# Performance work log

Hardware: AMD Instinct MI355X
Metric: run time of the kernel (lower is better)

## Reference

```python
import math
import jax, jax.numpy as jnp
import numpy as np

H = 16       # num_attention_heads
HD = 64      # head_size
D = H * HD   # hidden_size = 1024
B = 4
L = 1024
P = 2 * L - 1  # relative position length


def setup_inputs() -> dict:
    key = jax.random.key(0)
    ks = jax.random.split(key, 12)
    s = 0.02
    return {
        "hidden_states": jax.random.normal(ks[0], (B, L, D), jnp.float32),
        "relative_position_embeddings": jax.random.normal(ks[1], (1, P, D), jnp.float32),
        "Wq": jax.random.normal(ks[2], (D, D), jnp.float32) * s,
        "bq": jnp.zeros((D,), jnp.float32),
        "Wk": jax.random.normal(ks[3], (D, D), jnp.float32) * s,
        "bk": jnp.zeros((D,), jnp.float32),
        "Wv": jax.random.normal(ks[4], (D, D), jnp.float32) * s,
        "bv": jnp.zeros((D,), jnp.float32),
        "Wpos": jax.random.normal(ks[5], (D, D), jnp.float32) * s,  # linear_pos, no bias
        "pos_bias_u": jax.random.normal(ks[6], (H, HD), jnp.float32) * s,
        "pos_bias_v": jax.random.normal(ks[7], (H, HD), jnp.float32) * s,
        "Wo": jax.random.normal(ks[8], (D, D), jnp.float32) * s,
        "bo": jnp.zeros((D,), jnp.float32),
    }


def reference(hidden_states, relative_position_embeddings, Wq, bq, Wk, bk, Wv, bv,
              Wpos, pos_bias_u, pos_bias_v, Wo, bo):
    b, l, d = hidden_states.shape
    scale = 1.0 / math.sqrt(HD)

    # QKV projections -> [B, L, H, HD]
    q = (hidden_states @ Wq + bq).reshape(b, l, H, HD)
    k = (hidden_states @ Wk + bk).reshape(b, l, H, HD)
    v = (hidden_states @ Wv + bv).reshape(b, l, H, HD)

    # projected relative position embeddings -> [P, H, HD]
    pos = (relative_position_embeddings[0] @ Wpos).reshape(-1, H, HD)
    p = pos.shape[0]

    # Transformer-XL style content/position scores
    q_u = q + pos_bias_u  # [B, L, H, HD]
    q_v = q + pos_bias_v
    scores_ac = jnp.einsum('blhd,bmhd->bhlm', q_u, k)      # [B, H, L, L]
    scores_bd = jnp.einsum('blhd,phd->bhlp', q_v, pos)     # [B, H, L, P]

    # relative shift trick: pad one zero column, reshape, drop first row, re-slice
    zero_pad = jnp.zeros((b, H, l, 1), scores_bd.dtype)
    sbd = jnp.concatenate([zero_pad, scores_bd], axis=-1)  # [B, H, L, P+1]
    sbd = sbd.reshape(b, H, p + 1, l)[:, :, 1:]            # [B, H, P, L]
    sbd = sbd.reshape(b, H, l, p)[..., : p // 2 + 1]       # [B, H, L, L]

    scores = (scores_ac + sbd) * scale
    probs = jax.nn.softmax(scores, axis=-1)                # dropout p=0 (eval)

    ctx = jnp.einsum('bhlm,bmhd->blhd', probs, v).reshape(b, l, d)
    out = ctx @ Wo + bo
    return (out, probs)
```

## Files before the change

kernel.cpp:

```cpp
#include <hip/hip_runtime.h>
#include <hip/hip_bf16.h>

constexpr int H  = 16;
constexpr int HD = 64;
constexpr int D  = 1024;
constexpr int B  = 4;
constexpr int L  = 1024;
constexpr int P  = 2047;
constexpr int Pp = 2048;
constexpr int M  = B * L;
constexpr long OUT_ELEMS = (long)B * L * D;
constexpr float SCALE = 0.125f;

typedef __attribute__((ext_vector_type(8))) short  bf16x8;
typedef __attribute__((ext_vector_type(4))) float  f32x4;

#define MFMA(a, b, c) __builtin_amdgcn_mfma_f32_16x16x32_bf16((a), (b), (c), 0, 0, 0)

__device__ __forceinline__ unsigned short f2bf(float f) {
    __hip_bfloat16 h = __float2bfloat16(f);
    return __builtin_bit_cast(unsigned short, h);
}
__device__ __forceinline__ float bf2f(unsigned short u) {
    unsigned int v = ((unsigned int)u) << 16;
    return __builtin_bit_cast(float, v);
}

__global__ void cvt_kernel(const float* __restrict__ in, unsigned short* __restrict__ out,
                           long nvalid, long ntotal) {
    long i = ((long)blockIdx.x * blockDim.x + threadIdx.x) * 4;
    if (i >= ntotal) return;
    if (i < nvalid) {
        float4 v = *(const float4*)(in + i);
        out[i + 0] = f2bf(v.x);
        out[i + 1] = f2bf(v.y);
        out[i + 2] = f2bf(v.z);
        out[i + 3] = f2bf(v.w);
    } else {
        out[i + 0] = 0; out[i + 1] = 0; out[i + 2] = 0; out[i + 3] = 0;
    }
}

__global__ void wtrans_kernel(const float* __restrict__ W, unsigned short* __restrict__ Wt) {
    __shared__ float t[32][33];
    int n0 = blockIdx.x * 32, k0 = blockIdx.y * 32;
    int tx = threadIdx.x, ty = threadIdx.y;
#pragma unroll
    for (int s = 0; s < 4; ++s)
        t[ty + s * 8][tx] = W[(long)(k0 + ty + s * 8) * D + n0 + tx];
    __syncthreads();
#pragma unroll
    for (int s = 0; s < 4; ++s)
        Wt[(long)(n0 + ty + s * 8) * D + k0 + tx] = f2bf(t[tx][ty + s * 8]);
}

__global__ void vtrans_kernel(const unsigned short* __restrict__ Vb, unsigned short* __restrict__ Vt) {
    __shared__ unsigned short t[64][65];
    int b = blockIdx.z, h = blockIdx.y, l0 = blockIdx.x * 64;
    int tx = threadIdx.x & 63, ty = threadIdx.x >> 6;
#pragma unroll
    for (int s = 0; s < 16; ++s) {
        int l = s * 4 + ty;
        t[l][tx] = Vb[(long)(b * L + l0 + l) * D + h * HD + tx];
    }
    __syncthreads();
#pragma unroll
    for (int s = 0; s < 16; ++s) {
        int d = s * 4 + ty;
        Vt[(long)((b * H + h) * HD + d) * L + l0 + tx] = t[tx][d];
    }
}

template <int MODE>
__global__ __launch_bounds__(256) void gemm_bt(const unsigned short* __restrict__ A,
                                               const unsigned short* __restrict__ Bt,
                                               const float* __restrict__ bias,
                                               float* __restrict__ outF,
                                               unsigned short* __restrict__ outB) {
    int wave = threadIdx.x >> 6;
    int lane = threadIdx.x & 63;
    int r = lane & 15, g = lane >> 4;
    int row0 = blockIdx.x * 64 + wave * 16;
    int col0 = blockIdx.y * 64;
    f32x4 acc[4] = {};
    const long arow = (long)(row0 + r) * D;
    for (int ks = 0; ks < D; ks += 32) {
        bf16x8 a = *(const bf16x8*)(A + arow + ks + g * 8);
#pragma unroll
        for (int c = 0; c < 4; ++c) {
            bf16x8 b = *(const bf16x8*)(Bt + (long)(col0 + c * 16 + r) * D + ks + g * 8);
            acc[c] = MFMA(a, b, acc[c]);
        }
    }
#pragma unroll
    for (int c = 0; c < 4; ++c) {
        int col = col0 + c * 16 + r;
        float bv = (MODE != 2) ? bias[col] : 0.f;
#pragma unroll
        for (int i = 0; i < 4; ++i) {
            long row = row0 + g * 4 + i;
            float v = acc[c][i] + bv;
            if (MODE == 0) outF[row * D + col] = v;
            else           outB[row * D + col] = f2bf(v);
        }
    }
}

template <int OUT>
__device__ __forceinline__ void attn_sweep(
    int b, int h, int l0, int r, int g,
    const bf16x8* aqu, const bf16x8* aqv,
    const unsigned short* __restrict__ Kb, const unsigned short* __restrict__ posb,
    const unsigned short* __restrict__ Vt,
    float (*Es)[80], unsigned short* Ps,
    float* rsum, const float* inv, float* __restrict__ probs, f32x4* ctxacc)
{
    const long Srow0 = ((long)((b * H + h) * L + l0)) * L;
    for (int mc = 0; mc < L; mc += 64) {
        int rp0 = (L - 1) + mc - l0 - 15;
        f32x4 eacc[5];
#pragma unroll
        for (int t = 0; t < 5; ++t) eacc[t] = f32x4{0.f, 0.f, 0.f, 0.f};
#pragma unroll
        for (int ks = 0; ks < 2; ++ks)
#pragma unroll
            for (int t = 0; t < 5; ++t) {
                bf16x8 bp = *(const bf16x8*)(posb + (long)(rp0 + t * 16 + r) * D + h * HD + ks * 32 + g * 8);
                eacc[t] = MFMA(aqv[ks], bp, eacc[t]);
            }
#pragma unroll
        for (int t = 0; t < 5; ++t)
#pragma unroll
            for (int i = 0; i < 4; ++i)
                Es[g * 4 + i][t * 16 + r] = eacc[t][i];
        asm volatile("s_waitcnt lgkmcnt(0)" ::: "memory");
        __builtin_amdgcn_sched_barrier(0);

#pragma unroll
        for (int t = 0; t < 4; ++t) {
            f32x4 acc = {0.f, 0.f, 0.f, 0.f};
#pragma unroll
            for (int ks = 0; ks < 2; ++ks) {
                bf16x8 bk = *(const bf16x8*)(Kb + (long)(b * L + mc + t * 16 + r) * D + h * HD + ks * 32 + g * 8);
                acc = MFMA(aqu[ks], bk, acc);
            }
            int j = t * 16 + r;
#pragma unroll
            for (int i = 0; i < 4; ++i) {
                int il = g * 4 + i;
                float s = (acc[i] + Es[il][j - il + 15]) * SCALE;
                float e = __expf(s);
                if (OUT) {
                    float p = e * inv[i];
                    probs[Srow0 + (long)il * L + mc + j] = p;
                    int elem = il * 64 + j;
                    Ps[elem ^ ((il & 7) << 3)] = f2bf(p);
                } else {
                    rsum[i] += e;
                }
            }
        }
        if (OUT) {
            asm volatile("s_waitcnt lgkmcnt(0)" ::: "memory");
            __builtin_amdgcn_sched_barrier(0);
#pragma unroll
            for (int kh = 0; kh < 2; ++kh) {
                int elem = (r * 64 + kh * 32 + g * 8) ^ ((r & 7) << 3);
                bf16x8 pa = *(const bf16x8*)(Ps + elem);
#pragma unroll
                for (int c = 0; c < 4; ++c) {
                    bf16x8 bv = *(const bf16x8*)(Vt + (long)((b * H + h) * HD + c * 16 + r) * L + mc + kh * 32 + g * 8);
                    ctxacc[c] = MFMA(pa, bv, ctxacc[c]);
                }
            }
        }
        asm volatile("" ::: "memory");
    }
}

__global__ __launch_bounds__(256) void fused_attn(
    const unsigned short* __restrict__ Qb, const unsigned short* __restrict__ Kb,
    const unsigned short* __restrict__ posb, const float* __restrict__ pu,
    const float* __restrict__ pv, const unsigned short* __restrict__ Vt,
    float* __restrict__ probs, unsigned short* __restrict__ ctxb)
{
    __shared__ float Es[4][16][80];
    __shared__ unsigned short Ps[4][1024];
    int tid = threadIdx.x;
    int wave = tid >> 6, lane = tid & 63;
    int r = lane & 15, g = lane >> 4;

    int lin = blockIdx.x;
    int swz = (lin & 7) * 128 + (lin >> 3);
    int h = swz >> 6;
    int b = (swz >> 4) & 3;
    int l0 = (swz & 15) * 64 + wave * 16;

    bf16x8 aqu[2], aqv[2];
    long qoff = (long)(b * L + l0 + r) * D + h * HD;
#pragma unroll
    for (int ks = 0; ks < 2; ++ks) {
        bf16x8 q = *(const bf16x8*)(Qb + qoff + ks * 32 + g * 8);
        bf16x8 u, v;
#pragma unroll
        for (int e = 0; e < 8; ++e) {
            float qf = bf2f((unsigned short)q[e]);
            int d = ks * 32 + g * 8 + e;
            u[e] = (short)f2bf(qf + pu[h * HD + d]);
            v[e] = (short)f2bf(qf + pv[h * HD + d]);
        }
        aqu[ks] = u; aqv[ks] = v;
    }

    float rsum[4] = {0.f, 0.f, 0.f, 0.f};
    f32x4 ctxacc[4] = {};

    attn_sweep<0>(b, h, l0, r, g, aqu, aqv, Kb, posb, Vt,
                  Es[wave], Ps[wave], rsum, nullptr, probs, ctxacc);

    float inv[4];
#pragma unroll
    for (int i = 0; i < 4; ++i) {
        float s = rsum[i];
        for (int off = 1; off < 16; off <<= 1) s += __shfl_xor(s, off);
        inv[i] = 1.0f / s;
    }

    attn_sweep<1>(b, h, l0, r, g, aqu, aqv, Kb, posb, Vt,
                  Es[wave], Ps[wave], rsum, inv, probs, ctxacc);

#pragma unroll
    for (int c = 0; c < 4; ++c)
#pragma unroll
        for (int i = 0; i < 4; ++i)
            ctxb[(long)(b * L + l0 + g * 4 + i) * D + h * HD + c * 16 + r] = f2bf(ctxacc[c][i]);
}

extern "C" void kernel_launch(void* const* d_in, const int* in_sizes, int n_in,
                              void* d_out, int out_size, void* d_ws, size_t ws_size,
                              hipStream_t stream) {
    const float* hs   = (const float*)d_in[0];
    const float* rpe  = (const float*)d_in[1];
    const float* Wq   = (const float*)d_in[2];
    const float* bq   = (const float*)d_in[3];
    const float* Wk   = (const float*)d_in[4];
    const float* bk   = (const float*)d_in[5];
    const float* Wv   = (const float*)d_in[6];
    const float* bv   = (const float*)d_in[7];
    const float* Wpos = (const float*)d_in[8];
    const float* pu   = (const float*)d_in[9];
    const float* pv   = (const float*)d_in[10];
    const float* Wo   = (const float*)d_in[11];
    const float* bo   = (const float*)d_in[12];

    char* ws = (char*)d_ws;
    size_t off = 0;
    auto alloc = [&](size_t bytes) -> void* {
        void* p = ws + off;
        off += (bytes + 255) & ~(size_t)255;
        return p;
    };
    unsigned short* Xb   = (unsigned short*)alloc((size_t)M * D * 2);
    unsigned short* Wqt  = (unsigned short*)alloc((size_t)D * D * 2);
    unsigned short* Wkt  = (unsigned short*)alloc((size_t)D * D * 2);
    unsigned short* Wvt  = (unsigned short*)alloc((size_t)D * D * 2);
    unsigned short* Wpot = (unsigned short*)alloc((size_t)D * D * 2);
    unsigned short* Wot  = (unsigned short*)alloc((size_t)D * D * 2);
    unsigned short* rpb  = (unsigned short*)alloc((size_t)Pp * D * 2);
    unsigned short* posb = (unsigned short*)alloc((size_t)Pp * D * 2);
    unsigned short* Qb   = (unsigned short*)alloc((size_t)M * D * 2);
    unsigned short* Kb   = (unsigned short*)alloc((size_t)M * D * 2);
    unsigned short* Vb   = (unsigned short*)alloc((size_t)M * D * 2);
    unsigned short* Vt   = (unsigned short*)alloc((size_t)M * D * 2);
    unsigned short* ctxb = (unsigned short*)alloc((size_t)M * D * 2);

    float* outp  = (float*)d_out;
    float* probs = outp + OUT_ELEMS;

    cvt_kernel<<<(M * D) / 1024, 256, 0, stream>>>(hs, Xb, (long)M * D, (long)M * D);
    cvt_kernel<<<(Pp * D) / 1024, 256, 0, stream>>>(rpe, rpb, (long)P * D, (long)Pp * D);
    dim3 wtg(32, 32), wtb(32, 8);
    wtrans_kernel<<<wtg, wtb, 0, stream>>>(Wq, Wqt);
    wtrans_kernel<<<wtg, wtb, 0, stream>>>(Wk, Wkt);
    wtrans_kernel<<<wtg, wtb, 0, stream>>>(Wv, Wvt);
    wtrans_kernel<<<wtg, wtb, 0, stream>>>(Wpos, Wpot);
    wtrans_kernel<<<wtg, wtb, 0, stream>>>(Wo, Wot);

    gemm_bt<1><<<dim3(M / 64, D / 64), 256, 0, stream>>>(Xb, Wqt, bq, nullptr, Qb);
    gemm_bt<1><<<dim3(M / 64, D / 64), 256, 0, stream>>>(Xb, Wkt, bk, nullptr, Kb);
    gemm_bt<1><<<dim3(M / 64, D / 64), 256, 0, stream>>>(Xb, Wvt, bv, nullptr, Vb);
    gemm_bt<2><<<dim3(Pp / 64, D / 64), 256, 0, stream>>>(rpb, Wpot, nullptr, nullptr, posb);
    vtrans_kernel<<<dim3(L / 64, H, B), 256, 0, stream>>>(Vb, Vt);

    fused_attn<<<B * H * (L / 64), 256, 0, stream>>>(Qb, Kb, posb, pu, pv, Vt, probs, ctxb);

    gemm_bt<0><<<dim3(M / 64, D / 64), 256, 0, stream>>>(ctxb, Wot, bo, outp, nullptr);
}
```

Baseline: 1.036 ms.

## Split attention key range across four waves and cache exp values between passes

```diff
diff --git a/kernel.cpp b/kernel.cpp
--- a/kernel.cpp
+++ b/kernel.cpp
@@ -106,134 +106,184 @@
     }
 }
 
-template <int OUT>
-__device__ __forceinline__ void attn_sweep(
-    int b, int h, int l0, int r, int g,
-    const bf16x8* aqu, const bf16x8* aqv,
-    const unsigned short* __restrict__ Kb, const unsigned short* __restrict__ posb,
-    const unsigned short* __restrict__ Vt,
-    float (*Es)[80], unsigned short* Ps,
-    float* rsum, const float* inv, float* __restrict__ probs, f32x4* ctxacc)
-{
-    const long Srow0 = ((long)((b * H + h) * L + l0)) * L;
-    for (int mc = 0; mc < L; mc += 64) {
-        int rp0 = (L - 1) + mc - l0 - 15;
-        f32x4 eacc[5];
-#pragma unroll
-        for (int t = 0; t < 5; ++t) eacc[t] = f32x4{0.f, 0.f, 0.f, 0.f};
-#pragma unroll
-        for (int ks = 0; ks < 2; ++ks)
-#pragma unroll
-            for (int t = 0; t < 5; ++t) {
-                bf16x8 bp = *(const bf16x8*)(posb + (long)(rp0 + t * 16 + r) * D + h * HD + ks * 32 + g * 8);
-                eacc[t] = MFMA(aqv[ks], bp, eacc[t]);
-            }
-#pragma unroll
-        for (int t = 0; t < 5; ++t)
-#pragma unroll
-            for (int i = 0; i < 4; ++i)
-                Es[g * 4 + i][t * 16 + r] = eacc[t][i];
-        asm volatile("s_waitcnt lgkmcnt(0)" ::: "memory");
-        __builtin_amdgcn_sched_barrier(0);
-
-#pragma unroll
-        for (int t = 0; t < 4; ++t) {
-            f32x4 acc = {0.f, 0.f, 0.f, 0.f};
-#pragma unroll
-            for (int ks = 0; ks < 2; ++ks) {
-                bf16x8 bk = *(const bf16x8*)(Kb + (long)(b * L + mc + t * 16 + r) * D + h * HD + ks * 32 + g * 8);
-                acc = MFMA(aqu[ks], bk, acc);
-            }
-            int j = t * 16 + r;
-#pragma unroll
-            for (int i = 0; i < 4; ++i) {
-                int il = g * 4 + i;
-                float s = (acc[i] + Es[il][j - il + 15]) * SCALE;
-                float e = __expf(s);
-                if (OUT) {
-                    float p = e * inv[i];
-                    probs[Srow0 + (long)il * L + mc + j] = p;
-                    int elem = il * 64 + j;
-                    Ps[elem ^ ((il & 7) << 3)] = f2bf(p);
-                } else {
-                    rsum[i] += e;
-                }
-            }
-        }
-        if (OUT) {
-            asm volatile("s_waitcnt lgkmcnt(0)" ::: "memory");
-            __builtin_amdgcn_sched_barrier(0);
-#pragma unroll
-            for (int kh = 0; kh < 2; ++kh) {
-                int elem = (r * 64 + kh * 32 + g * 8) ^ ((r & 7) << 3);
-                bf16x8 pa = *(const bf16x8*)(Ps + elem);
-#pragma unroll
-                for (int c = 0; c < 4; ++c) {
-                    bf16x8 bv = *(const bf16x8*)(Vt + (long)((b * H + h) * HD + c * 16 + r) * L + mc + kh * 32 + g * 8);
-                    ctxacc[c] = MFMA(pa, bv, ctxacc[c]);
-                }
-            }
-        }
-        asm volatile("" ::: "memory");
-    }
-}
-
-__global__ __launch_bounds__(256) void fused_attn(
+__global__ __launch_bounds__(1024, 4) void fused_attn(
     const unsigned short* __restrict__ Qb, const unsigned short* __restrict__ Kb,
     const unsigned short* __restrict__ posb, const float* __restrict__ pu,
     const float* __restrict__ pv, const unsigned short* __restrict__ Vt,
     float* __restrict__ probs, unsigned short* __restrict__ ctxb)
 {
-    __shared__ float Es[4][16][80];
-    __shared__ unsigned short Ps[4][1024];
+    __shared__ __align__(16) unsigned short scratch[16][1600];
+    __shared__ __align__(16) float rs[64][4];
+    __shared__ __align__(16) float ctxcomb[4][16][68];
+
     int tid = threadIdx.x;
     int wave = tid >> 6, lane = tid & 63;
     int r = lane & 15, g = lane >> 4;
+    int wq = wave & 3, wr = wave >> 2;
 
     int lin = blockIdx.x;
     int swz = (lin & 7) * 128 + (lin >> 3);
     int h = swz >> 6;
     int b = (swz >> 4) & 3;
-    int l0 = (swz & 15) * 64 + wave * 16;
+    int l0base = (swz & 15) * 64;
+    int l0 = l0base + wr * 16;
+
+    unsigned short* Es = scratch[wave];
+    unsigned short* Ps = scratch[wave];
+    const int hHD = h * HD;
 
     bf16x8 aqu[2], aqv[2];
-    long qoff = (long)(b * L + l0 + r) * D + h * HD;
-#pragma unroll
-    for (int ks = 0; ks < 2; ++ks) {
-        bf16x8 q = *(const bf16x8*)(Qb + qoff + ks * 32 + g * 8);
-        bf16x8 u, v;
-#pragma unroll
-        for (int e = 0; e < 8; ++e) {
-            float qf = bf2f((unsigned short)q[e]);
-            int d = ks * 32 + g * 8 + e;
-            u[e] = (short)f2bf(qf + pu[h * HD + d]);
-            v[e] = (short)f2bf(qf + pv[h * HD + d]);
-        }
-        aqu[ks] = u; aqv[ks] = v;
+    {
+        long qoff = (long)(b * L + l0 + r) * D + hHD;
+#pragma unroll
+        for (int ks = 0; ks < 2; ++ks) {
+            bf16x8 q = *(const bf16x8*)(Qb + qoff + ks * 32 + g * 8);
+            bf16x8 u, v;
+#pragma unroll
+            for (int e = 0; e < 8; ++e) {
+                float qf = bf2f((unsigned short)q[e]);
+                int d = ks * 32 + g * 8 + e;
+                u[e] = (short)f2bf(qf + pu[hHD + d]);
+                v[e] = (short)f2bf(qf + pv[hHD + d]);
+            }
+            aqu[ks] = u; aqv[ks] = v;
+        }
     }
 
     float rsum[4] = {0.f, 0.f, 0.f, 0.f};
-    f32x4 ctxacc[4] = {};
-
-    attn_sweep<0>(b, h, l0, r, g, aqu, aqv, Kb, posb, Vt,
-                  Es[wave], Ps[wave], rsum, nullptr, probs, ctxacc);
-
-    float inv[4];
+    unsigned int pPk[4][4][2];
+    const long KbRow = (long)(b * L) * D + hHD;
+
+#pragma unroll
+    for (int cc = 0; cc < 4; ++cc) {
+        int mc = wq * 256 + cc * 64;
+        int rp0 = (L - 1) + mc - l0 - 15;
+        f32x4 eacc[5] = {};
+#pragma unroll
+        for (int ks = 0; ks < 2; ++ks)
+#pragma unroll
+            for (int t = 0; t < 5; ++t) {
+                bf16x8 bp = *(const bf16x8*)(posb + (long)(rp0 + t * 16 + r) * D + hHD + ks * 32 + g * 8);
+                eacc[t] = MFMA(aqv[ks], bp, eacc[t]);
+            }
+#pragma unroll
+        for (int t = 0; t < 5; ++t) {
+            ushort4 pk;
+            pk.x = f2bf(eacc[t][0]); pk.y = f2bf(eacc[t][1]);
+            pk.z = f2bf(eacc[t][2]); pk.w = f2bf(eacc[t][3]);
+            *(ushort4*)(Es + (t * 16 + r) * 20 + g * 4) = pk;
+        }
+        asm volatile("s_waitcnt lgkmcnt(0)" ::: "memory");
+        __builtin_amdgcn_sched_barrier(0);
+
+#pragma unroll
+        for (int t = 0; t < 4; ++t) {
+            f32x4 acc = {};
+#pragma unroll
+            for (int ks = 0; ks < 2; ++ks) {
+                bf16x8 bk = *(const bf16x8*)(Kb + KbRow + (long)(mc + t * 16 + r) * D + ks * 32 + g * 8);
+                acc = MFMA(aqu[ks], bk, acc);
+            }
+            float ev[4];
+#pragma unroll
+            for (int i = 0; i < 4; ++i) {
+                int il = g * 4 + i;
+                int c = t * 16 + r - il + 15;
+                float s = (acc[i] + bf2f(Es[c * 20 + il])) * SCALE;
+                float e = __expf(s);
+                rsum[i] += e;
+                ev[i] = e;
+            }
+            pPk[cc][t][0] = ((unsigned)f2bf(ev[1]) << 16) | f2bf(ev[0]);
+            pPk[cc][t][1] = ((unsigned)f2bf(ev[3]) << 16) | f2bf(ev[2]);
+        }
+        asm volatile("" ::: "memory");
+    }
+
 #pragma unroll
     for (int i = 0; i < 4; ++i) {
         float s = rsum[i];
-        for (int off = 1; off < 16; off <<= 1) s += __shfl_xor(s, off);
-        inv[i] = 1.0f / s;
-    }
-
-    attn_sweep<1>(b, h, l0, r, g, aqu, aqv, Kb, posb, Vt,
-                  Es[wave], Ps[wave], rsum, inv, probs, ctxacc);
-
-#pragma unroll
-    for (int c = 0; c < 4; ++c)
-#pragma unroll
-        for (int i = 0; i < 4; ++i)
-            ctxb[(long)(b * L + l0 + g * 4 + i) * D + h * HD + c * 16 + r] = f2bf(ctxacc[c][i]);
+        s += __shfl_xor(s, 1); s += __shfl_xor(s, 2);
+        s += __shfl_xor(s, 4); s += __shfl_xor(s, 8);
+        rsum[i] = s;
+    }
+    if (r == 0) {
+#pragma unroll
+        for (int i = 0; i < 4; ++i) rs[wr * 16 + g * 4 + i][wq] = rsum[i];
+    }
+    __syncthreads();
+    float inv[4];
+#pragma unroll
+    for (int i = 0; i < 4; ++i) {
+        float4 v = *(const float4*)&rs[wr * 16 + g * 4 + i][0];
+        inv[i] = 1.0f / (v.x + v.y + v.z + v.w);
+    }
+
+    f32x4 ctxacc[4] = {};
+    const long ProwBase = ((long)((b * H + h) * L + l0)) * L;
+    const long VtBase = (long)((b * H + h) * HD) * L;
+#pragma unroll
+    for (int cc = 0; cc < 4; ++cc) {
+        int mc = wq * 256 + cc * 64;
+#pragma unroll
+        for (int t = 0; t < 4; ++t) {
+            float ev[4];
+            ev[0] = bf2f((unsigned short)(pPk[cc][t][0] & 0xffff));
+            ev[1] = bf2f((unsigned short)(pPk[cc][t][0] >> 16));
+            ev[2] = bf2f((unsigned short)(pPk[cc][t][1] & 0xffff));
+            ev[3] = bf2f((unsigned short)(pPk[cc][t][1] >> 16));
+#pragma unroll
+            for (int i = 0; i < 4; ++i) {
+                int il = g * 4 + i;
+                int j = t * 16 + r;
+                float p = ev[i] * inv[i];
+                probs[ProwBase + (long)il * L + mc + j] = p;
+                int elem = il * 64 + j;
+                Ps[elem ^ ((il & 7) << 3)] = f2bf(p);
+            }
+        }
+        asm volatile("s_waitcnt lgkmcnt(0)" ::: "memory");
+        __builtin_amdgcn_sched_barrier(0);
+#pragma unroll
+        for (int kh = 0; kh < 2; ++kh) {
+            int elem = (r * 64 + kh * 32 + g * 8) ^ ((r & 7) << 3);
+            bf16x8 pa = *(const bf16x8*)(Ps + elem);
+#pragma unroll
+            for (int c = 0; c < 4; ++c) {
+                bf16x8 bv = *(const bf16x8*)(Vt + VtBase + (long)(c * 16 + r) * L + mc + kh * 32 + g * 8);
+                ctxacc[c] = MFMA(pa, bv, ctxacc[c]);
+            }
+        }
+        asm volatile("" ::: "memory");
+    }
+
+    if (wq == 0) {
+#pragma unroll
+        for (int c = 0; c < 4; ++c)
+#pragma unroll
+            for (int i = 0; i < 4; ++i)
+                ctxcomb[wr][g * 4 + i][c * 16 + r] = ctxacc[c][i];
+    }
+    __syncthreads();
+#pragma unroll
+    for (int q = 1; q < 4; ++q) {
+        if (wq == q) {
+#pragma unroll
+            for (int c = 0; c < 4; ++c)
+#pragma unroll
+                for (int i = 0; i < 4; ++i)
+                    ctxcomb[wr][g * 4 + i][c * 16 + r] += ctxacc[c][i];
+        }
+        __syncthreads();
+    }
+    {
+        int row = lane >> 2;
+        int colg = (lane & 3) * 4;
+        float4 v = *(const float4*)&ctxcomb[wr][row][wq * 16 + colg];
+        ushort4 o;
+        o.x = f2bf(v.x); o.y = f2bf(v.y); o.z = f2bf(v.z); o.w = f2bf(v.w);
+        *(ushort4*)(ctxb + (long)(b * L + l0base + wr * 16 + row) * D + hHD + wq * 16 + colg) = o;
+    }
 }
 
 extern "C" void kernel_launch(void* const* d_in, const int* in_sizes, int n_in,
@@ -292,7 +342,7 @@
     gemm_bt<2><<<dim3(Pp / 64, D / 64), 256, 0, stream>>>(rpb, Wpot, nullptr, nullptr, posb);
     vtrans_kernel<<<dim3(L / 64, H, B), 256, 0, stream>>>(Vb, Vt);
 
-    fused_attn<<<B * H * (L / 64), 256, 0, stream>>>(Qb, Kb, posb, pu, pv, Vt, probs, ctxb);
+    fused_attn<<<B * H * (L / 64), 1024, 0, stream>>>(Qb, Kb, posb, pu, pv, Vt, probs, ctxb);
 
     gemm_bt<0><<<dim3(M / 64, D / 64), 256, 0, stream>>>(ctxb, Wot, bo, outp, nullptr);
 }
```

Result: faster. 861.1 us (-16.9%).
